# Kernel optimization log

Hardware: AMD Instinct MI355X
Metric: run time of the kernel (lower is better)

## Reference

```python
import jax, jax.numpy as jnp
import numpy as np

N_HEAD = 8
HIDDEN = 512
HEAD_DIM = HIDDEN // N_HEAD
EPS = 1e-5


def _layernorm(x, g, b):
    mu = jnp.mean(x, axis=-1, keepdims=True)
    var = jnp.var(x, axis=-1, keepdims=True)
    return (x - mu) * jax.lax.rsqrt(var + EPS) * g + b


def setup_inputs() -> dict:
    key = jax.random.key(0)
    ks = jax.random.split(key, 12)
    s = 1.0 / np.sqrt(HIDDEN)
    x = jax.random.normal(ks[0], (4, 2048, HIDDEN), dtype=jnp.float32)
    # per-head Q/K/V projections stacked: [H, D, dh] weights, [H, dh] biases
    Wq = jax.random.uniform(ks[1], (N_HEAD, HIDDEN, HEAD_DIM), minval=-s, maxval=s, dtype=jnp.float32)
    bq = jax.random.uniform(ks[2], (N_HEAD, HEAD_DIM), minval=-s, maxval=s, dtype=jnp.float32)
    Wk = jax.random.uniform(ks[3], (N_HEAD, HIDDEN, HEAD_DIM), minval=-s, maxval=s, dtype=jnp.float32)
    bk = jax.random.uniform(ks[4], (N_HEAD, HEAD_DIM), minval=-s, maxval=s, dtype=jnp.float32)
    Wv = jax.random.uniform(ks[5], (N_HEAD, HIDDEN, HEAD_DIM), minval=-s, maxval=s, dtype=jnp.float32)
    bv = jax.random.uniform(ks[6], (N_HEAD, HEAD_DIM), minval=-s, maxval=s, dtype=jnp.float32)
    Wm = jax.random.uniform(ks[7], (HIDDEN, HIDDEN), minval=-s, maxval=s, dtype=jnp.float32)
    bm = jax.random.uniform(ks[8], (HIDDEN,), minval=-s, maxval=s, dtype=jnp.float32)
    Wo = jax.random.uniform(ks[9], (HIDDEN, HIDDEN), minval=-s, maxval=s, dtype=jnp.float32)
    bo = jax.random.uniform(ks[10], (HIDDEN,), minval=-s, maxval=s, dtype=jnp.float32)
    g1 = jnp.ones((HIDDEN,), jnp.float32); b1 = jnp.zeros((HIDDEN,), jnp.float32)
    g2 = jnp.ones((HIDDEN,), jnp.float32); b2 = jnp.zeros((HIDDEN,), jnp.float32)
    return {"x": x, "g1": g1, "b1": b1, "Wq": Wq, "bq": bq, "Wk": Wk, "bk": bk,
            "Wv": Wv, "bv": bv, "Wm": Wm, "bm": bm, "g2": g2, "b2": b2, "Wo": Wo, "bo": bo}


def reference(x, g1, b1, Wq, bq, Wk, bk, Wv, bv, Wm, bm, g2, b2, Wo, bo):
    h = _layernorm(x, g1, b1)                                 # [B,S,D]
    # stacked per-head projections: [B,H,S,dh]
    q = jnp.einsum('bsd,hde->bhse', h, Wq) + bq[None, :, None, :]
    k = jnp.einsum('bsd,hde->bhse', h, Wk) + bk[None, :, None, :]
    v = jnp.einsum('bsd,hde->bhse', h, Wv) + bv[None, :, None, :]
    scores = jnp.einsum('bhse,bhte->bhst', q, k) / jnp.sqrt(jnp.float32(HEAD_DIM))
    attn = jax.nn.softmax(scores, axis=-1)                    # [B,H,S,S]
    out = jnp.einsum('bhst,bhte->bhse', attn, v)              # [B,H,S,dh]
    B, H, S, E = out.shape
    out_mha = jnp.transpose(out, (0, 2, 1, 3)).reshape(B, S, H * E)  # concat heads
    h_ln_post = out_mha @ Wm + bm + x
    h_fc = _layernorm(h_ln_post, g2, b2)
    return jax.nn.relu(h_fc @ Wo + bo) + h_ln_post
```

## Files before the change

kernel.cpp:

```cpp
#include <hip/hip_runtime.h>
#include <hip/hip_bf16.h>


typedef __attribute__((ext_vector_type(8))) short bf16x8;
typedef __attribute__((ext_vector_type(4))) float f32x4;
typedef __attribute__((ext_vector_type(16))) float f32x16;
typedef __attribute__((ext_vector_type(8))) unsigned short u16x8;

typedef union { bf16x8 v; unsigned u[4]; u16x8 s; } frag_u;

typedef const unsigned int __attribute__((address_space(1)))* gas_t;
typedef unsigned int __attribute__((address_space(3)))* las_t;
static __device__ __forceinline__ void glds16(const void* g, void* l) {
    __builtin_amdgcn_global_load_lds((gas_t)g, (las_t)l, 16, 0, 0);
}

static __device__ __forceinline__ unsigned short f2b(float f) {
    union { float f; unsigned u; } a; a.f = f;
    unsigned r = a.u + 0x7FFFu + ((a.u >> 16) & 1u);
    return (unsigned short)(r >> 16);
}
static __device__ __forceinline__ float b2f(unsigned short u) {
    union { unsigned u; float f; } c; c.u = ((unsigned)u) << 16; return c.f;
}
static __device__ __forceinline__ unsigned pack_bf16(float lo, float hi) {
    __hip_bfloat162 p = __float22bfloat162_rn(make_float2(lo, hi));
    unsigned r; __builtin_memcpy(&r, &p, 4); return r;
}
static __device__ __forceinline__ void swap32(int hi, unsigned a, unsigned b,
                                              unsigned& x, unsigned& y) {
#if __has_builtin(__builtin_amdgcn_permlane32_swap)
    typedef __attribute__((ext_vector_type(2))) int i32x2;
    i32x2 r = __builtin_amdgcn_permlane32_swap((int)a, (int)b, false, false);
    x = (unsigned)r[0]; y = (unsigned)r[1];
#else
    unsigned ta = (unsigned)__shfl_xor((int)a, 32);
    unsigned tb = (unsigned)__shfl_xor((int)b, 32);
    x = hi ? tb : a;
    y = hi ? b : ta;
#endif
}

__global__ __launch_bounds__(256) void prep_weights_k(
    const float* __restrict__ Wq, const float* __restrict__ Wk, const float* __restrict__ Wv,
    const float* __restrict__ Wm, const float* __restrict__ Wo,
    unsigned short* __restrict__ wqT, unsigned short* __restrict__ wkT,
    unsigned short* __restrict__ wvT, unsigned short* __restrict__ wmT,
    unsigned short* __restrict__ woT)
{
    int idx = blockIdx.x * 256 + threadIdx.x;
    int n = idx >> 9, k = idx & 511;
    int h = n >> 6, e = n & 63;
    size_t src_qkv = ((size_t)h * 512 + k) * 64 + e;
    wqT[idx] = f2b(Wq[src_qkv]);
    wkT[idx] = f2b(Wk[src_qkv]);
    wvT[idx] = f2b(Wv[src_qkv]);
    wmT[idx] = f2b(Wm[(size_t)k * 512 + n]);
    woT[idx] = f2b(Wo[(size_t)k * 512 + n]);
}

__global__ __launch_bounds__(64) void ln_bf16_k(
    const float* __restrict__ X, const float* __restrict__ gam,
    const float* __restrict__ bet, unsigned short* __restrict__ O)
{
    int row = blockIdx.x, lane = threadIdx.x;
    const float4* xr = (const float4*)(X + (size_t)row * 512);
    float4 v0 = xr[lane * 2], v1 = xr[lane * 2 + 1];
    float vv[8] = {v0.x, v0.y, v0.z, v0.w, v1.x, v1.y, v1.z, v1.w};
    float s = 0.f, s2 = 0.f;
    #pragma unroll
    for (int j = 0; j < 8; ++j) { s += vv[j]; s2 += vv[j] * vv[j]; }
    #pragma unroll
    for (int d = 1; d < 64; d <<= 1) { s += __shfl_xor(s, d); s2 += __shfl_xor(s2, d); }
    float mean = s * (1.0f / 512.0f);
    float var  = s2 * (1.0f / 512.0f) - mean * mean;
    float rstd = rsqrtf(var + 1e-5f);
    int c = lane * 8;
    u16x8 o;
    #pragma unroll
    for (int j = 0; j < 8; ++j) o[j] = f2b((vv[j] - mean) * rstd * gam[c + j] + bet[c + j]);
    *(u16x8*)(O + (size_t)row * 512 + c) = o;
}

__global__ __launch_bounds__(256) void gemm_qkv_k(
    const unsigned short* __restrict__ A, const unsigned short* __restrict__ Bt,
    const float* __restrict__ bq, const float* __restrict__ bk, const float* __restrict__ bv,
    unsigned short* __restrict__ Qo, unsigned short* __restrict__ Ko,
    unsigned short* __restrict__ VtO)
{
    __shared__ unsigned short Al[128 * 32];
    __shared__ unsigned short Bl[128 * 32];
    int tid = threadIdx.x;
    int wid = tid >> 6, lane = tid & 63;
    int lr = lane & 15, lg = lane >> 4;
    int m0 = blockIdx.x * 128, n0 = blockIdx.y * 128;
    int seg = blockIdx.y >> 2;
    int wr = (wid >> 1) * 64, wc = (wid & 1) * 64;
    f32x4 acc[4][4] = {};
    const unsigned short* Ag = A  + (size_t)(m0 + wid * 32 + (lane >> 2)) * 512 + (lane & 3) * 8;
    const unsigned short* Bg = Bt + (size_t)(n0 + wid * 32 + (lane >> 2)) * 512 + (lane & 3) * 8;
    unsigned short* Alw = Al + wid * 32 * 32;
    unsigned short* Blw = Bl + wid * 32 * 32;
    for (int k0 = 0; k0 < 512; k0 += 32) {
        __syncthreads();
        glds16(Ag + k0,             Alw);
        glds16(Ag + k0 + 16 * 512,  Alw + 16 * 32);
        glds16(Bg + k0,             Blw);
        glds16(Bg + k0 + 16 * 512,  Blw + 16 * 32);
        __syncthreads();
        bf16x8 af[4], bfr[4];
        #pragma unroll
        for (int m = 0; m < 4; ++m) af[m]  = *(const bf16x8*)(Al + (wr + m * 16 + lr) * 32 + lg * 8);
        #pragma unroll
        for (int n = 0; n < 4; ++n) bfr[n] = *(const bf16x8*)(Bl + (wc + n * 16 + lr) * 32 + lg * 8);
        #pragma unroll
        for (int m = 0; m < 4; ++m)
            #pragma unroll
            for (int n = 0; n < 4; ++n)
                acc[m][n] = __builtin_amdgcn_mfma_f32_16x16x32_bf16(af[m], bfr[n], acc[m][n], 0, 0, 0);
    }
    const float* bb = seg == 0 ? bq : (seg == 1 ? bk : bv);
    unsigned short* dst = seg == 0 ? Qo : Ko;
    #pragma unroll
    for (int m = 0; m < 4; ++m)
      #pragma unroll
      for (int n = 0; n < 4; ++n) {
        int gr0 = m0 + wr + m * 16 + 4 * lg;
        int nc  = ((blockIdx.y & 3) << 7) + wc + n * 16 + lr;
        float bias = bb[nc];
        if (seg < 2) {
            #pragma unroll
            for (int j = 0; j < 4; ++j)
                dst[(size_t)(gr0 + j) * 512 + nc] = f2b(acc[m][n][j] + bias);
        } else {
            int bbk = gr0 >> 11, ss = gr0 & 2047, hh = nc >> 6, ee = nc & 63;
            ushort4 pv;
            pv.x = f2b(acc[m][n][0] + bias);
            pv.y = f2b(acc[m][n][1] + bias);
            pv.z = f2b(acc[m][n][2] + bias);
            pv.w = f2b(acc[m][n][3] + bias);
            *(ushort4*)&VtO[((size_t)((bbk * 8 + hh) * 64 + ee) << 11) + ss] = pv;
        }
      }
}

template<int MODE>
__global__ __launch_bounds__(256) void gemm_n64_k(
    const unsigned short* __restrict__ A, const unsigned short* __restrict__ Bt,
    const float* __restrict__ bias, const float* __restrict__ aux,
    float* __restrict__ Cout)
{
    __shared__ unsigned short Al[128 * 32];
    __shared__ unsigned short Bl[64 * 32];
    int tid = threadIdx.x;
    int wid = tid >> 6, lane = tid & 63;
    int lr = lane & 15, lg = lane >> 4;
    int m0 = blockIdx.x * 128, n0 = blockIdx.y * 64;
    int wr = wid * 32;
    f32x4 acc[2][4] = {};
    const unsigned short* Ag = A  + (size_t)(m0 + wid * 32 + (lane >> 2)) * 512 + (lane & 3) * 8;
    const unsigned short* Bg = Bt + (size_t)(n0 + wid * 16 + (lane >> 2)) * 512 + (lane & 3) * 8;
    unsigned short* Alw = Al + wid * 32 * 32;
    unsigned short* Blw = Bl + wid * 16 * 32;
    for (int k0 = 0; k0 < 512; k0 += 32) {
        __syncthreads();
        glds16(Ag + k0,            Alw);
        glds16(Ag + k0 + 16 * 512, Alw + 16 * 32);
        glds16(Bg + k0,            Blw);
        __syncthreads();
        bf16x8 af[2], bfr[4];
        #pragma unroll
        for (int m = 0; m < 2; ++m) af[m]  = *(const bf16x8*)(Al + (wr + m * 16 + lr) * 32 + lg * 8);
        #pragma unroll
        for (int n = 0; n < 4; ++n) bfr[n] = *(const bf16x8*)(Bl + (n * 16 + lr) * 32 + lg * 8);
        #pragma unroll
        for (int m = 0; m < 2; ++m)
            #pragma unroll
            for (int n = 0; n < 4; ++n)
                acc[m][n] = __builtin_amdgcn_mfma_f32_16x16x32_bf16(af[m], bfr[n], acc[m][n], 0, 0, 0);
    }
    #pragma unroll
    for (int m = 0; m < 2; ++m)
      #pragma unroll
      for (int n = 0; n < 4; ++n)
        #pragma unroll
        for (int j = 0; j < 4; ++j) {
            int gr = m0 + wr + m * 16 + 4 * lg + j;
            int gc = n0 + n * 16 + lr;
            float v = acc[m][n][j] + bias[gc];
            if (MODE == 3) v = v > 0.0f ? v : 0.0f;
            Cout[(size_t)gr * 512 + gc] = v + aux[(size_t)gr * 512 + gc];
        }
}

__global__ __launch_bounds__(128, 2) void attn7_k(
    const unsigned short* __restrict__ Q, const unsigned short* __restrict__ K,
    const unsigned short* __restrict__ Vt, unsigned short* __restrict__ O)
{
    __shared__ __align__(16) unsigned short Kl[2][4096];
    __shared__ __align__(16) unsigned short Vl[2][4096];

    const int tid  = threadIdx.x;
    const int lane = tid & 63;
    const int q31  = lane & 31;
    const int hi   = lane >> 5;
    const int wid  = tid >> 6;

    int bid = blockIdx.x;
    int xcd = bid & 7, idx = bid >> 3;
    int bh  = xcd + 8 * (idx >> 5);
    int qt  = idx & 31;
    int b = bh >> 3, h = bh & 7;
    int q0 = qt * 64 + wid * 32;

    const unsigned short* Qb = Q  + (size_t)b * 2048 * 512 + h * 64;
    const unsigned short* Kb = K  + (size_t)b * 2048 * 512 + h * 64;
    const unsigned short* Vb = Vt + (size_t)(b * 8 + h) * 64 * 2048;

    frag_u qf[4];
    const float qs = 0.125f * 1.44269504f;
    #pragma unroll
    for (int ds = 0; ds < 4; ++ds) {
        u16x8 raw = *(const u16x8*)(Qb + (size_t)(q0 + q31) * 512 + ds * 16 + hi * 8);
        #pragma unroll
        for (int i = 0; i < 4; ++i)
            qf[ds].u[i] = pack_bf16(b2f(raw[2 * i]) * qs, b2f(raw[2 * i + 1]) * qs);
    }

    frag_u onesf;
    #pragma unroll
    for (int i = 0; i < 4; ++i) onesf.u[i] = 0x3F803F80u;

    unsigned lws[8];
    #pragma unroll
    for (int s = 0; s < 8; ++s)
        lws[s] = (unsigned)((lane & 31) * 256 + (((lane >> 5) * 128 + s * 16) ^ ((lane & 15) << 4)));

    u16x8 st[8];
    auto LOADT = [&](int t0) {
        if (wid == 0) {
            const unsigned short* p = Kb + (size_t)(t0 + lane) * 512;
            #pragma unroll
            for (int s = 0; s < 8; ++s) st[s] = *(const u16x8*)(p + s * 8);
        } else {
            const unsigned short* p = Vb + (size_t)lane * 2048 + t0;
            #pragma unroll
            for (int s = 0; s < 8; ++s) st[s] = *(const u16x8*)(p + s * 8);
        }
    };

    f32x16 acc0, acc1, lacc;
    #pragma unroll
    for (int r = 0; r < 16; ++r) { acc0[r] = 0.0f; acc1[r] = 0.0f; lacc[r] = 0.0f; }
    const int swz = (q31 & 15) << 4;

    LOADT(0);
    {
        char* mb = (wid == 0) ? (char*)Kl[0] : (char*)Vl[0];
        #pragma unroll
        for (int s = 0; s < 8; ++s) *(u16x8*)(mb + lws[s]) = st[s];
    }
    LOADT(64);
    __syncthreads();

    int cur = 0;
    for (int it = 0; it < 32; ++it) {
        if (it < 31) {
            char* mb = (wid == 0) ? (char*)Kl[cur ^ 1] : (char*)Vl[cur ^ 1];
            #pragma unroll
            for (int s = 0; s < 8; ++s) *(u16x8*)(mb + lws[s]) = st[s];
        }
        if (it < 30) LOADT((it + 2) * 64);

        const char* Kh = (const char*)Kl[cur];
        const char* Vh = (const char*)Vl[cur];

        f32x16 s0, s1;
        #pragma unroll
        for (int r = 0; r < 16; ++r) { s0[r] = 0.0f; s1[r] = 0.0f; }
        __builtin_amdgcn_s_setprio(1);
        #pragma unroll
        for (int ds = 0; ds < 4; ++ds) {
            bf16x8 k0 = *(const bf16x8*)(Kh + q31 * 256 + ((ds * 32 + hi * 16) ^ swz));
            bf16x8 k1 = *(const bf16x8*)(Kh + q31 * 256 + ((128 + ds * 32 + hi * 16) ^ swz));
            s0 = __builtin_amdgcn_mfma_f32_32x32x16_bf16(k0, qf[ds].v, s0, 0, 0, 0);
            s1 = __builtin_amdgcn_mfma_f32_32x32x16_bf16(k1, qf[ds].v, s1, 0, 0, 0);
        }
        __builtin_amdgcn_s_setprio(0);

        #pragma unroll
        for (int r = 0; r < 16; ++r) {
            s0[r] = exp2f(s0[r]);
            s1[r] = exp2f(s1[r]);
        }

        frag_u pa[4];
        #pragma unroll
        for (int g = 0; g < 2; ++g) {
            unsigned A0 = pack_bf16(s0[8 * g + 0], s0[8 * g + 1]);
            unsigned A1 = pack_bf16(s0[8 * g + 2], s0[8 * g + 3]);
            unsigned A2 = pack_bf16(s0[8 * g + 4], s0[8 * g + 5]);
            unsigned A3 = pack_bf16(s0[8 * g + 6], s0[8 * g + 7]);
            swap32(hi, A0, A2, pa[g].u[0], pa[g].u[2]);
            swap32(hi, A1, A3, pa[g].u[1], pa[g].u[3]);
            unsigned B0 = pack_bf16(s1[8 * g + 0], s1[8 * g + 1]);
            unsigned B1 = pack_bf16(s1[8 * g + 2], s1[8 * g + 3]);
            unsigned B2 = pack_bf16(s1[8 * g + 4], s1[8 * g + 5]);
            unsigned B3 = pack_bf16(s1[8 * g + 6], s1[8 * g + 7]);
            swap32(hi, B0, B2, pa[2 + g].u[0], pa[2 + g].u[2]);
            swap32(hi, B1, B3, pa[2 + g].u[1], pa[2 + g].u[3]);
        }

        __builtin_amdgcn_s_setprio(1);
        #pragma unroll
        for (int ks = 0; ks < 4; ++ks) {
            bf16x8 v0 = *(const bf16x8*)(Vh + q31 * 256 + ((ks * 32 + hi * 16) ^ swz));
            bf16x8 v1 = *(const bf16x8*)(Vh + q31 * 256 + ((128 + ks * 32 + hi * 16) ^ swz));
            acc0 = __builtin_amdgcn_mfma_f32_32x32x16_bf16(pa[ks].v, v0, acc0, 0, 0, 0);
            acc1 = __builtin_amdgcn_mfma_f32_32x32x16_bf16(pa[ks].v, v1, acc1, 0, 0, 0);
            lacc = __builtin_amdgcn_mfma_f32_32x32x16_bf16(pa[ks].v, onesf.v, lacc, 0, 0, 0);
        }
        __builtin_amdgcn_s_setprio(0);

        __syncthreads();
        cur ^= 1;
    }

    #pragma unroll
    for (int r = 0; r < 16; ++r) {
        int cr = (r & 3) + 8 * (r >> 2) + 4 * hi;
        float li = 1.0f / lacc[r];
        size_t rowoff = (size_t)(b * 2048 + q0 + cr) * 512 + h * 64 + q31;
        O[rowoff]      = f2b(acc0[r] * li);
        O[rowoff + 32] = f2b(acc1[r] * li);
    }
}

extern "C" void kernel_launch(void* const* d_in, const int* in_sizes, int n_in,
                              void* d_out, int out_size, void* d_ws, size_t ws_size,
                              hipStream_t stream)
{
    const float* x  = (const float*)d_in[0];
    const float* g1 = (const float*)d_in[1];
    const float* b1 = (const float*)d_in[2];
    const float* Wq = (const float*)d_in[3];
    const float* bq = (const float*)d_in[4];
    const float* Wk = (const float*)d_in[5];
    const float* bk = (const float*)d_in[6];
    const float* Wv = (const float*)d_in[7];
    const float* bv = (const float*)d_in[8];
    const float* Wm = (const float*)d_in[9];
    const float* bm = (const float*)d_in[10];
    const float* g2 = (const float*)d_in[11];
    const float* b2 = (const float*)d_in[12];
    const float* Wo = (const float*)d_in[13];
    const float* bo = (const float*)d_in[14];
    float* out = (float*)d_out;

    char* ws = (char*)d_ws;
    const size_t EB = (size_t)8192 * 512 * 2;
    unsigned short* h1  = (unsigned short*)(ws);
    unsigned short* qb  = (unsigned short*)(ws + EB);
    unsigned short* kb  = (unsigned short*)(ws + 2 * EB);
    unsigned short* vtb = (unsigned short*)(ws + 3 * EB);
    unsigned short* ao  = (unsigned short*)(ws + 4 * EB);
    unsigned short* h2  = (unsigned short*)(ws + 5 * EB);
    float*          hlp = (float*)(ws + 6 * EB);
    unsigned short* wqT = (unsigned short*)(ws + 8 * EB);
    unsigned short* wkT = wqT + 512 * 512;
    unsigned short* wvT = wkT + 512 * 512;
    unsigned short* wmT = wvT + 512 * 512;
    unsigned short* woT = wmT + 512 * 512;

    prep_weights_k<<<1024, 256, 0, stream>>>(Wq, Wk, Wv, Wm, Wo, wqT, wkT, wvT, wmT, woT);
    ln_bf16_k<<<8192, 64, 0, stream>>>(x, g1, b1, h1);
    gemm_qkv_k<<<dim3(64, 12), 256, 0, stream>>>(h1, wqT, bq, bk, bv, qb, kb, vtb);
    attn7_k<<<1024, 128, 0, stream>>>(qb, kb, vtb, ao);
    gemm_n64_k<2><<<dim3(64, 8), 256, 0, stream>>>(ao, wmT, bm, x, hlp);
    ln_bf16_k<<<8192, 64, 0, stream>>>(hlp, g2, b2, h2);
    gemm_n64_k<3><<<dim3(64, 8), 256, 0, stream>>>(h2, woT, bo, hlp, out);
}
```

Before: 147.2 us.

## Split attention key range across two wave pairs and merge partials in LDS

The attention kernel now runs 4 waves per block. Two query sub-tiles are each processed by two waves, and each wave handles half of the 2048-key range. Each half loads its own K/V tiles, and the partial output and row-sum accumulators are combined through shared memory at the end. Double buffering is replaced by single-buffered staging with two barriers per iteration. exp2f is swapped for the hardware exp2 builtin. The aim is more parallelism per query tile and more waves in flight. In exchange it adds barriers, a reduction step and extra register and LDS use, which may limit occupancy.

```diff
diff --git a/kernel.cpp b/kernel.cpp
--- a/kernel.cpp
+++ b/kernel.cpp
@@ -26,6 +26,13 @@
 static __device__ __forceinline__ unsigned pack_bf16(float lo, float hi) {
     __hip_bfloat162 p = __float22bfloat162_rn(make_float2(lo, hi));
     unsigned r; __builtin_memcpy(&r, &p, 4); return r;
+}
+static __device__ __forceinline__ float fexp2(float x) {
+#if __has_builtin(__builtin_amdgcn_exp2f)
+    return __builtin_amdgcn_exp2f(x);
+#else
+    return exp2f(x);
+#endif
 }
 static __device__ __forceinline__ void swap32(int hi, unsigned a, unsigned b,
                                               unsigned& x, unsigned& y) {
@@ -193,25 +200,25 @@
         }
 }
 
-__global__ __launch_bounds__(128, 2) void attn7_k(
+__global__ __launch_bounds__(256, 4) void attn8_k(
     const unsigned short* __restrict__ Q, const unsigned short* __restrict__ K,
     const unsigned short* __restrict__ Vt, unsigned short* __restrict__ O)
 {
-    __shared__ __align__(16) unsigned short Kl[2][4096];
-    __shared__ __align__(16) unsigned short Vl[2][4096];
+    __shared__ __align__(16) char smem[32768];
 
     const int tid  = threadIdx.x;
     const int lane = tid & 63;
     const int q31  = lane & 31;
     const int hi   = lane >> 5;
     const int wid  = tid >> 6;
+    const int qsub = wid >> 1, half = wid & 1;
 
     int bid = blockIdx.x;
     int xcd = bid & 7, idx = bid >> 3;
     int bh  = xcd + 8 * (idx >> 5);
     int qt  = idx & 31;
     int b = bh >> 3, h = bh & 7;
-    int q0 = qt * 64 + wid * 32;
+    int q0 = qt * 64 + qsub * 32;
 
     const unsigned short* Qb = Q  + (size_t)b * 2048 * 512 + h * 64;
     const unsigned short* Kb = K  + (size_t)b * 2048 * 512 + h * 64;
@@ -236,14 +243,18 @@
     for (int s = 0; s < 8; ++s)
         lws[s] = (unsigned)((lane & 31) * 256 + (((lane >> 5) * 128 + s * 16) ^ ((lane & 15) << 4)));
 
+    char* stage_base = smem + (qsub ? 16384 : 0) + half * 8192;
+    const char* Kh = smem + half * 8192;
+    const char* Vh = smem + 16384 + half * 8192;
+
     u16x8 st[8];
-    auto LOADT = [&](int t0) {
-        if (wid == 0) {
-            const unsigned short* p = Kb + (size_t)(t0 + lane) * 512;
+    auto LOADT = [&](int it) {
+        if (qsub == 0) {
+            const unsigned short* p = Kb + (size_t)(half * 1024 + it * 64 + lane) * 512;
             #pragma unroll
             for (int s = 0; s < 8; ++s) st[s] = *(const u16x8*)(p + s * 8);
         } else {
-            const unsigned short* p = Vb + (size_t)lane * 2048 + t0;
+            const unsigned short* p = Vb + (size_t)lane * 2048 + half * 1024 + it * 64;
             #pragma unroll
             for (int s = 0; s < 8; ++s) st[s] = *(const u16x8*)(p + s * 8);
         }
@@ -255,25 +266,12 @@
     const int swz = (q31 & 15) << 4;
 
     LOADT(0);
-    {
-        char* mb = (wid == 0) ? (char*)Kl[0] : (char*)Vl[0];
-        #pragma unroll
-        for (int s = 0; s < 8; ++s) *(u16x8*)(mb + lws[s]) = st[s];
-    }
-    LOADT(64);
-    __syncthreads();
-
-    int cur = 0;
-    for (int it = 0; it < 32; ++it) {
-        if (it < 31) {
-            char* mb = (wid == 0) ? (char*)Kl[cur ^ 1] : (char*)Vl[cur ^ 1];
-            #pragma unroll
-            for (int s = 0; s < 8; ++s) *(u16x8*)(mb + lws[s]) = st[s];
-        }
-        if (it < 30) LOADT((it + 2) * 64);
-
-        const char* Kh = (const char*)Kl[cur];
-        const char* Vh = (const char*)Vl[cur];
+    for (int it = 0; it < 16; ++it) {
+        __syncthreads();
+        #pragma unroll
+        for (int s = 0; s < 8; ++s) *(u16x8*)(stage_base + lws[s]) = st[s];
+        if (it < 15) LOADT(it + 1);
+        __syncthreads();
 
         f32x16 s0, s1;
         #pragma unroll
@@ -290,8 +288,8 @@
 
         #pragma unroll
         for (int r = 0; r < 16; ++r) {
-            s0[r] = exp2f(s0[r]);
-            s1[r] = exp2f(s1[r]);
+            s0[r] = fexp2(s0[r]);
+            s1[r] = fexp2(s1[r]);
         }
 
         frag_u pa[4];
@@ -321,18 +319,37 @@
             lacc = __builtin_amdgcn_mfma_f32_32x32x16_bf16(pa[ks].v, onesf.v, lacc, 0, 0, 0);
         }
         __builtin_amdgcn_s_setprio(0);
-
-        __syncthreads();
-        cur ^= 1;
-    }
-
-    #pragma unroll
-    for (int r = 0; r < 16; ++r) {
-        int cr = (r & 3) + 8 * (r >> 2) + 4 * hi;
-        float li = 1.0f / lacc[r];
-        size_t rowoff = (size_t)(b * 2048 + q0 + cr) * 512 + h * 64 + q31;
-        O[rowoff]      = f2b(acc0[r] * li);
-        O[rowoff + 32] = f2b(acc1[r] * li);
+    }
+
+    __syncthreads();
+    float* mq = (float*)smem + (size_t)qsub * (64 * 48) + (size_t)lane * 48;
+    if (half == 1) {
+        #pragma unroll
+        for (int u = 0; u < 4; ++u) {
+            *(f32x4*)(mq + 4 * u) =
+                (f32x4){acc0[4*u], acc0[4*u+1], acc0[4*u+2], acc0[4*u+3]};
+            *(f32x4*)(mq + 16 + 4 * u) =
+                (f32x4){acc1[4*u], acc1[4*u+1], acc1[4*u+2], acc1[4*u+3]};
+            *(f32x4*)(mq + 32 + 4 * u) =
+                (f32x4){lacc[4*u], lacc[4*u+1], lacc[4*u+2], lacc[4*u+3]};
+        }
+    }
+    __syncthreads();
+    if (half == 0) {
+        #pragma unroll
+        for (int r = 0; r < 16; ++r) {
+            acc0[r] += mq[r];
+            acc1[r] += mq[16 + r];
+            lacc[r] += mq[32 + r];
+        }
+        #pragma unroll
+        for (int r = 0; r < 16; ++r) {
+            int cr = (r & 3) + 8 * (r >> 2) + 4 * hi;
+            float li = 1.0f / lacc[r];
+            size_t rowoff = (size_t)(b * 2048 + q0 + cr) * 512 + h * 64 + q31;
+            O[rowoff]      = f2b(acc0[r] * li);
+            O[rowoff + 32] = f2b(acc1[r] * li);
+        }
     }
 }
 
@@ -375,7 +392,7 @@
     prep_weights_k<<<1024, 256, 0, stream>>>(Wq, Wk, Wv, Wm, Wo, wqT, wkT, wvT, wmT, woT);
     ln_bf16_k<<<8192, 64, 0, stream>>>(x, g1, b1, h1);
     gemm_qkv_k<<<dim3(64, 12), 256, 0, stream>>>(h1, wqT, bq, bk, bv, qb, kb, vtb);
-    attn7_k<<<1024, 128, 0, stream>>>(qb, kb, vtb, ao);
+    attn8_k<<<1024, 256, 0, stream>>>(qb, kb, vtb, ao);
     gemm_n64_k<2><<<dim3(64, 8), 256, 0, stream>>>(ao, wmT, bm, x, hlp);
     ln_bf16_k<<<8192, 64, 0, stream>>>(hlp, g2, b2, h2);
     gemm_n64_k<3><<<dim3(64, 8), 256, 0, stream>>>(h2, woT, bo, hlp, out);
```

Result: slower. 228.4 us (+55.1%).

## Split attention KV range across two waves, load K/V directly to registers

Applied to the files above, without the earlier changes.

The attention kernel is rebuilt so each block handles 32 query rows, with its two waves splitting the key range in half and merging partial outputs and row sums through shared memory at the end. K and V tiles are now loaded straight from global memory into register fragments with register double-buffering, replacing the LDS staging and the per-iteration block barrier. The row-sum MFMA against a ones vector is replaced by VALU adds plus a cross-lane shuffle, and exp2f becomes the hardware exp2 builtin. The grid doubles to 2048 blocks to raise parallelism. In exchange, each K/V element is now read from global/L2 once per block rather than shared via LDS, which raises cache traffic, and more live registers may lower occupancy.

```diff
diff --git a/kernel.cpp b/kernel.cpp
--- a/kernel.cpp
+++ b/kernel.cpp
@@ -26,6 +26,13 @@
 static __device__ __forceinline__ unsigned pack_bf16(float lo, float hi) {
     __hip_bfloat162 p = __float22bfloat162_rn(make_float2(lo, hi));
     unsigned r; __builtin_memcpy(&r, &p, 4); return r;
+}
+static __device__ __forceinline__ float fexp2(float x) {
+#if __has_builtin(__builtin_amdgcn_exp2f)
+    return __builtin_amdgcn_exp2f(x);
+#else
+    return exp2f(x);
+#endif
 }
 static __device__ __forceinline__ void swap32(int hi, unsigned a, unsigned b,
                                               unsigned& x, unsigned& y) {
@@ -193,25 +200,24 @@
         }
 }
 
-__global__ __launch_bounds__(128, 2) void attn7_k(
+__global__ __launch_bounds__(128) void attn10_k(
     const unsigned short* __restrict__ Q, const unsigned short* __restrict__ K,
     const unsigned short* __restrict__ Vt, unsigned short* __restrict__ O)
 {
-    __shared__ __align__(16) unsigned short Kl[2][4096];
-    __shared__ __align__(16) unsigned short Vl[2][4096];
+    __shared__ __align__(16) float mrg[64 * 34];
 
     const int tid  = threadIdx.x;
     const int lane = tid & 63;
     const int q31  = lane & 31;
     const int hi   = lane >> 5;
-    const int wid  = tid >> 6;
+    const int half = tid >> 6;
 
     int bid = blockIdx.x;
-    int xcd = bid & 7, idx = bid >> 3;
-    int bh  = xcd + 8 * (idx >> 5);
-    int qt  = idx & 31;
+    int xcd = bid & 7, r0 = bid >> 3;
+    int bh  = (r0 >> 6) * 8 + xcd;
+    int qt  = r0 & 63;
     int b = bh >> 3, h = bh & 7;
-    int q0 = qt * 64 + wid * 32;
+    int q0 = qt * 32;
 
     const unsigned short* Qb = Q  + (size_t)b * 2048 * 512 + h * 64;
     const unsigned short* Kb = K  + (size_t)b * 2048 * 512 + h * 64;
@@ -227,112 +233,88 @@
             qf[ds].u[i] = pack_bf16(b2f(raw[2 * i]) * qs, b2f(raw[2 * i + 1]) * qs);
     }
 
-    frag_u onesf;
-    #pragma unroll
-    for (int i = 0; i < 4; ++i) onesf.u[i] = 0x3F803F80u;
-
-    unsigned lws[8];
-    #pragma unroll
-    for (int s = 0; s < 8; ++s)
-        lws[s] = (unsigned)((lane & 31) * 256 + (((lane >> 5) * 128 + s * 16) ^ ((lane & 15) << 4)));
-
-    u16x8 st[8];
-    auto LOADT = [&](int t0) {
-        if (wid == 0) {
-            const unsigned short* p = Kb + (size_t)(t0 + lane) * 512;
-            #pragma unroll
-            for (int s = 0; s < 8; ++s) st[s] = *(const u16x8*)(p + s * 8);
-        } else {
-            const unsigned short* p = Vb + (size_t)lane * 2048 + t0;
-            #pragma unroll
-            for (int s = 0; s < 8; ++s) st[s] = *(const u16x8*)(p + s * 8);
+    const unsigned short* Kp = Kb + (size_t)(half * 1024 + q31) * 512 + hi * 8;
+    const unsigned short* Vp0 = Vb + (size_t)q31 * 2048        + half * 1024 + hi * 8;
+    const unsigned short* Vp1 = Vb + (size_t)(q31 + 32) * 2048 + half * 1024 + hi * 8;
+
+    f32x16 acc0, acc1;
+    #pragma unroll
+    for (int r = 0; r < 16; ++r) { acc0[r] = 0.0f; acc1[r] = 0.0f; }
+    float l_run = 0.0f;
+
+    frag_u kfA[4], kfB[4], vfA[4], vfB[4];
+    #define LOADK(dst, t0) { \
+        const unsigned short* kp_ = Kp + (size_t)(t0) * 512; \
+        dst[0].s = *(const u16x8*)(kp_);      dst[1].s = *(const u16x8*)(kp_ + 16); \
+        dst[2].s = *(const u16x8*)(kp_ + 32); dst[3].s = *(const u16x8*)(kp_ + 48); }
+    #define LOADV(dst, t0) { \
+        dst[0].s = *(const u16x8*)(Vp0 + (t0));      dst[1].s = *(const u16x8*)(Vp0 + (t0) + 16); \
+        dst[2].s = *(const u16x8*)(Vp1 + (t0));      dst[3].s = *(const u16x8*)(Vp1 + (t0) + 16); }
+
+    #define TILE(kf, vf)  { \
+        f32x16 s;                                                              \
+        _Pragma("unroll") for (int r = 0; r < 16; ++r) s[r] = 0.0f;            \
+        __builtin_amdgcn_s_setprio(1);                                         \
+        _Pragma("unroll") for (int ds = 0; ds < 4; ++ds)                       \
+            s = __builtin_amdgcn_mfma_f32_32x32x16_bf16(kf[ds].v, qf[ds].v, s, 0, 0, 0); \
+        __builtin_amdgcn_s_setprio(0);                                         \
+        _Pragma("unroll") for (int r = 0; r < 16; ++r) s[r] = fexp2(s[r]);     \
+        float ts = 0.0f;                                                       \
+        _Pragma("unroll") for (int r = 0; r < 16; ++r) ts += s[r];             \
+        l_run += ts + __shfl_xor(ts, 32);                                      \
+        frag_u pa0, pa1;                                                       \
+        {                                                                      \
+            unsigned A0 = pack_bf16(s[0], s[1]),  A1 = pack_bf16(s[2], s[3]);  \
+            unsigned A2 = pack_bf16(s[4], s[5]),  A3 = pack_bf16(s[6], s[7]);  \
+            swap32(hi, A0, A2, pa0.u[0], pa0.u[2]);                            \
+            swap32(hi, A1, A3, pa0.u[1], pa0.u[3]);                            \
+            unsigned B0 = pack_bf16(s[8], s[9]),  B1 = pack_bf16(s[10], s[11]);\
+            unsigned B2 = pack_bf16(s[12], s[13]),B3 = pack_bf16(s[14], s[15]);\
+            swap32(hi, B0, B2, pa1.u[0], pa1.u[2]);                            \
+            swap32(hi, B1, B3, pa1.u[1], pa1.u[3]);                            \
+        }                                                                      \
+        __builtin_amdgcn_s_setprio(1);                                         \
+        acc0 = __builtin_amdgcn_mfma_f32_32x32x16_bf16(pa0.v, vf[0].v, acc0, 0, 0, 0); \
+        acc0 = __builtin_amdgcn_mfma_f32_32x32x16_bf16(pa1.v, vf[1].v, acc0, 0, 0, 0); \
+        acc1 = __builtin_amdgcn_mfma_f32_32x32x16_bf16(pa0.v, vf[2].v, acc1, 0, 0, 0); \
+        acc1 = __builtin_amdgcn_mfma_f32_32x32x16_bf16(pa1.v, vf[3].v, acc1, 0, 0, 0); \
+        __builtin_amdgcn_s_setprio(0);                                         }
+
+    LOADK(kfA, 0); LOADV(vfA, 0);
+    for (int it = 0; it < 32; it += 2) {
+        int tB = (it + 1) * 32;
+        int tA = it + 2 < 32 ? (it + 2) * 32 : 0;
+        LOADK(kfB, tB); LOADV(vfB, tB);
+        TILE(kfA, vfA);
+        LOADK(kfA, tA); LOADV(vfA, tA);
+        TILE(kfB, vfB);
+    }
+    #undef LOADK
+    #undef LOADV
+    #undef TILE
+
+    float* mq = mrg + (size_t)lane * 34;
+    if (half == 1) {
+        #pragma unroll
+        for (int u = 0; u < 4; ++u) {
+            *(f32x4*)(mq + 4 * u)      = (f32x4){acc0[4*u], acc0[4*u+1], acc0[4*u+2], acc0[4*u+3]};
+            *(f32x4*)(mq + 16 + 4 * u) = (f32x4){acc1[4*u], acc1[4*u+1], acc1[4*u+2], acc1[4*u+3]};
         }
-    };
-
-    f32x16 acc0, acc1, lacc;
-    #pragma unroll
-    for (int r = 0; r < 16; ++r) { acc0[r] = 0.0f; acc1[r] = 0.0f; lacc[r] = 0.0f; }
-    const int swz = (q31 & 15) << 4;
-
-    LOADT(0);
-    {
-        char* mb = (wid == 0) ? (char*)Kl[0] : (char*)Vl[0];
-        #pragma unroll
-        for (int s = 0; s < 8; ++s) *(u16x8*)(mb + lws[s]) = st[s];
-    }
-    LOADT(64);
+        mq[32] = l_run;
+    }
     __syncthreads();
-
-    int cur = 0;
-    for (int it = 0; it < 32; ++it) {
-        if (it < 31) {
-            char* mb = (wid == 0) ? (char*)Kl[cur ^ 1] : (char*)Vl[cur ^ 1];
-            #pragma unroll
-            for (int s = 0; s < 8; ++s) *(u16x8*)(mb + lws[s]) = st[s];
+    if (half == 0) {
+        #pragma unroll
+        for (int r = 0; r < 16; ++r) { acc0[r] += mq[r]; acc1[r] += mq[16 + r]; }
+        float linv = 1.0f / (l_run + mq[32]);
+        #pragma unroll
+        for (int r = 0; r < 16; ++r) {
+            int cr = (r & 3) + 8 * (r >> 2) + 4 * hi;
+            float li = __shfl(linv, cr);
+            size_t rowoff = (size_t)(b * 2048 + q0 + cr) * 512 + h * 64 + q31;
+            O[rowoff]      = f2b(acc0[r] * li);
+            O[rowoff + 32] = f2b(acc1[r] * li);
         }
-        if (it < 30) LOADT((it + 2) * 64);
-
-        const char* Kh = (const char*)Kl[cur];
-        const char* Vh = (const char*)Vl[cur];
-
-        f32x16 s0, s1;
-        #pragma unroll
-        for (int r = 0; r < 16; ++r) { s0[r] = 0.0f; s1[r] = 0.0f; }
-        __builtin_amdgcn_s_setprio(1);
-        #pragma unroll
-        for (int ds = 0; ds < 4; ++ds) {
-            bf16x8 k0 = *(const bf16x8*)(Kh + q31 * 256 + ((ds * 32 + hi * 16) ^ swz));
-            bf16x8 k1 = *(const bf16x8*)(Kh + q31 * 256 + ((128 + ds * 32 + hi * 16) ^ swz));
-            s0 = __builtin_amdgcn_mfma_f32_32x32x16_bf16(k0, qf[ds].v, s0, 0, 0, 0);
-            s1 = __builtin_amdgcn_mfma_f32_32x32x16_bf16(k1, qf[ds].v, s1, 0, 0, 0);
-        }
-        __builtin_amdgcn_s_setprio(0);
-
-        #pragma unroll
-        for (int r = 0; r < 16; ++r) {
-            s0[r] = exp2f(s0[r]);
-            s1[r] = exp2f(s1[r]);
-        }
-
-        frag_u pa[4];
-        #pragma unroll
-        for (int g = 0; g < 2; ++g) {
-            unsigned A0 = pack_bf16(s0[8 * g + 0], s0[8 * g + 1]);
-            unsigned A1 = pack_bf16(s0[8 * g + 2], s0[8 * g + 3]);
-            unsigned A2 = pack_bf16(s0[8 * g + 4], s0[8 * g + 5]);
-            unsigned A3 = pack_bf16(s0[8 * g + 6], s0[8 * g + 7]);
-            swap32(hi, A0, A2, pa[g].u[0], pa[g].u[2]);
-            swap32(hi, A1, A3, pa[g].u[1], pa[g].u[3]);
-            unsigned B0 = pack_bf16(s1[8 * g + 0], s1[8 * g + 1]);
-            unsigned B1 = pack_bf16(s1[8 * g + 2], s1[8 * g + 3]);
-            unsigned B2 = pack_bf16(s1[8 * g + 4], s1[8 * g + 5]);
-            unsigned B3 = pack_bf16(s1[8 * g + 6], s1[8 * g + 7]);
-            swap32(hi, B0, B2, pa[2 + g].u[0], pa[2 + g].u[2]);
-            swap32(hi, B1, B3, pa[2 + g].u[1], pa[2 + g].u[3]);
-        }
-
-        __builtin_amdgcn_s_setprio(1);
-        #pragma unroll
-        for (int ks = 0; ks < 4; ++ks) {
-            bf16x8 v0 = *(const bf16x8*)(Vh + q31 * 256 + ((ks * 32 + hi * 16) ^ swz));
-            bf16x8 v1 = *(const bf16x8*)(Vh + q31 * 256 + ((128 + ks * 32 + hi * 16) ^ swz));
-            acc0 = __builtin_amdgcn_mfma_f32_32x32x16_bf16(pa[ks].v, v0, acc0, 0, 0, 0);
-            acc1 = __builtin_amdgcn_mfma_f32_32x32x16_bf16(pa[ks].v, v1, acc1, 0, 0, 0);
-            lacc = __builtin_amdgcn_mfma_f32_32x32x16_bf16(pa[ks].v, onesf.v, lacc, 0, 0, 0);
-        }
-        __builtin_amdgcn_s_setprio(0);
-
-        __syncthreads();
-        cur ^= 1;
-    }
-
-    #pragma unroll
-    for (int r = 0; r < 16; ++r) {
-        int cr = (r & 3) + 8 * (r >> 2) + 4 * hi;
-        float li = 1.0f / lacc[r];
-        size_t rowoff = (size_t)(b * 2048 + q0 + cr) * 512 + h * 64 + q31;
-        O[rowoff]      = f2b(acc0[r] * li);
-        O[rowoff + 32] = f2b(acc1[r] * li);
     }
 }
 
@@ -375,7 +357,7 @@
     prep_weights_k<<<1024, 256, 0, stream>>>(Wq, Wk, Wv, Wm, Wo, wqT, wkT, wvT, wmT, woT);
     ln_bf16_k<<<8192, 64, 0, stream>>>(x, g1, b1, h1);
     gemm_qkv_k<<<dim3(64, 12), 256, 0, stream>>>(h1, wqT, bq, bk, bv, qb, kb, vtb);
-    attn7_k<<<1024, 128, 0, stream>>>(qb, kb, vtb, ao);
+    attn10_k<<<2048, 128, 0, stream>>>(qb, kb, vtb, ao);
     gemm_n64_k<2><<<dim3(64, 8), 256, 0, stream>>>(ao, wmT, bm, x, hlp);
     ln_bf16_k<<<8192, 64, 0, stream>>>(hlp, g2, b2, h2);
     gemm_n64_k<3><<<dim3(64, 8), 256, 0, stream>>>(h2, woT, bo, hlp, out);
```

Measured after the change: 203.6 us. 38.3% more time.

## Stage attention K/V tiles with direct global-to-LDS loads and unrolled double buffer

Applied to the files above, without the earlier changes.

The attention kernel now loads K and V tiles straight from global memory into LDS with global_load_lds. This replaces the register staging followed by swizzled LDS stores, and the per-lane source offsets are precomputed so the existing XOR-swizzled LDS read pattern is kept. The main loop is unrolled by two over named A/B buffers, and exp2f is swapped for the hardware exp2 builtin. The min-blocks hint in launch_bounds is dropped, which may change register allocation and occupancy. The change also relies on the implicit wait at __syncthreads covering the asynchronous LDS loads.

```diff
diff --git a/kernel.cpp b/kernel.cpp
--- a/kernel.cpp
+++ b/kernel.cpp
@@ -26,6 +26,13 @@
 static __device__ __forceinline__ unsigned pack_bf16(float lo, float hi) {
     __hip_bfloat162 p = __float22bfloat162_rn(make_float2(lo, hi));
     unsigned r; __builtin_memcpy(&r, &p, 4); return r;
+}
+static __device__ __forceinline__ float fexp2(float x) {
+#if __has_builtin(__builtin_amdgcn_exp2f)
+    return __builtin_amdgcn_exp2f(x);
+#else
+    return exp2f(x);
+#endif
 }
 static __device__ __forceinline__ void swap32(int hi, unsigned a, unsigned b,
                                               unsigned& x, unsigned& y) {
@@ -193,12 +200,12 @@
         }
 }
 
-__global__ __launch_bounds__(128, 2) void attn7_k(
+__global__ __launch_bounds__(128) void attn12_k(
     const unsigned short* __restrict__ Q, const unsigned short* __restrict__ K,
     const unsigned short* __restrict__ Vt, unsigned short* __restrict__ O)
 {
-    __shared__ __align__(16) unsigned short Kl[2][4096];
-    __shared__ __align__(16) unsigned short Vl[2][4096];
+    __shared__ __align__(16) unsigned short KlA[4096], KlB[4096];
+    __shared__ __align__(16) unsigned short VlA[4096], VlB[4096];
 
     const int tid  = threadIdx.x;
     const int lane = tid & 63;
@@ -231,22 +238,23 @@
     #pragma unroll
     for (int i = 0; i < 4; ++i) onesf.u[i] = 0x3F803F80u;
 
-    unsigned lws[8];
-    #pragma unroll
-    for (int s = 0; s < 8; ++s)
-        lws[s] = (unsigned)((lane & 31) * 256 + (((lane >> 5) * 128 + s * 16) ^ ((lane & 15) << 4)));
-
-    u16x8 st[8];
-    auto LOADT = [&](int t0) {
-        if (wid == 0) {
-            const unsigned short* p = Kb + (size_t)(t0 + lane) * 512;
-            #pragma unroll
-            for (int s = 0; s < 8; ++s) st[s] = *(const u16x8*)(p + s * 8);
-        } else {
-            const unsigned short* p = Vb + (size_t)lane * 2048 + t0;
-            #pragma unroll
-            for (int s = 0; s < 8; ++s) st[s] = *(const u16x8*)(p + s * 8);
-        }
+    unsigned soff[8];
+    #pragma unroll
+    for (int j = 0; j < 8; ++j) {
+        int row31 = j * 4 + (lane >> 4);
+        int x = (lane & 15) ^ (row31 & 15);
+        int t = 32 * (x >> 3) + row31;
+        int s = x & 7;
+        soff[j] = (wid == 0) ? (unsigned)(t * 512 + s * 8)
+                             : (unsigned)(t * 2048 + s * 8);
+    }
+    const unsigned short* Gb = (wid == 0) ? Kb : Vb;
+
+    auto STAGE = [&](unsigned short* buf, int t0) {
+        const unsigned short* g = Gb + (wid == 0 ? (size_t)t0 * 512 : (size_t)t0);
+        #pragma unroll
+        for (int j = 0; j < 8; ++j)
+            glds16(g + soff[j], buf + j * 512);
     };
 
     f32x16 acc0, acc1, lacc;
@@ -254,27 +262,9 @@
     for (int r = 0; r < 16; ++r) { acc0[r] = 0.0f; acc1[r] = 0.0f; lacc[r] = 0.0f; }
     const int swz = (q31 & 15) << 4;
 
-    LOADT(0);
-    {
-        char* mb = (wid == 0) ? (char*)Kl[0] : (char*)Vl[0];
-        #pragma unroll
-        for (int s = 0; s < 8; ++s) *(u16x8*)(mb + lws[s]) = st[s];
-    }
-    LOADT(64);
-    __syncthreads();
-
-    int cur = 0;
-    for (int it = 0; it < 32; ++it) {
-        if (it < 31) {
-            char* mb = (wid == 0) ? (char*)Kl[cur ^ 1] : (char*)Vl[cur ^ 1];
-            #pragma unroll
-            for (int s = 0; s < 8; ++s) *(u16x8*)(mb + lws[s]) = st[s];
-        }
-        if (it < 30) LOADT((it + 2) * 64);
-
-        const char* Kh = (const char*)Kl[cur];
-        const char* Vh = (const char*)Vl[cur];
-
+    auto COMPUTE = [&](const unsigned short* Kh_, const unsigned short* Vh_) {
+        const char* Kh = (const char*)Kh_;
+        const char* Vh = (const char*)Vh_;
         f32x16 s0, s1;
         #pragma unroll
         for (int r = 0; r < 16; ++r) { s0[r] = 0.0f; s1[r] = 0.0f; }
@@ -290,8 +280,8 @@
 
         #pragma unroll
         for (int r = 0; r < 16; ++r) {
-            s0[r] = exp2f(s0[r]);
-            s1[r] = exp2f(s1[r]);
+            s0[r] = fexp2(s0[r]);
+            s1[r] = fexp2(s1[r]);
         }
 
         frag_u pa[4];
@@ -321,9 +311,19 @@
             lacc = __builtin_amdgcn_mfma_f32_32x32x16_bf16(pa[ks].v, onesf.v, lacc, 0, 0, 0);
         }
         __builtin_amdgcn_s_setprio(0);
-
-        __syncthreads();
-        cur ^= 1;
+    };
+
+    STAGE(wid == 0 ? KlA : VlA, 0);
+    __syncthreads();
+
+    #pragma unroll 1
+    for (int it = 0; it < 32; it += 2) {
+        if (it + 1 < 32) STAGE(wid == 0 ? KlB : VlB, (it + 1) * 64);
+        COMPUTE(KlA, VlA);
+        __syncthreads();
+        if (it + 2 < 32) STAGE(wid == 0 ? KlA : VlA, (it + 2) * 64);
+        COMPUTE(KlB, VlB);
+        __syncthreads();
     }
 
     #pragma unroll
@@ -375,7 +375,7 @@
     prep_weights_k<<<1024, 256, 0, stream>>>(Wq, Wk, Wv, Wm, Wo, wqT, wkT, wvT, wmT, woT);
     ln_bf16_k<<<8192, 64, 0, stream>>>(x, g1, b1, h1);
     gemm_qkv_k<<<dim3(64, 12), 256, 0, stream>>>(h1, wqT, bq, bk, bv, qb, kb, vtb);
-    attn7_k<<<1024, 128, 0, stream>>>(qb, kb, vtb, ao);
+    attn12_k<<<1024, 128, 0, stream>>>(qb, kb, vtb, ao);
     gemm_n64_k<2><<<dim3(64, 8), 256, 0, stream>>>(ao, wmT, bm, x, hlp);
     ln_bf16_k<<<8192, 64, 0, stream>>>(hlp, g2, b2, h2);
     gemm_n64_k<3><<<dim3(64, 8), 256, 0, stream>>>(h2, woT, bo, hlp, out);
```

Result: faster. 133.4 us (-9.4%).
